# Kernel tuning notes

Measured on AMD Instinct MI355X. Metric: run time of the kernel, lower is better.

## Reference

```python
import jax, jax.numpy as jnp
import numpy as np

DIM = 256
DH = 32
HEADS = DIM // DH
AG = 6      # agent_size
WS = 7      # window_size
N = AG * WS * WS  # 294 tokens per window


def _rel_index():
    ws = (AG, WS, WS)
    coords = np.stack(np.meshgrid(np.arange(ws[0]), np.arange(ws[1]), np.arange(ws[2]), indexing='ij'))
    flat = coords.reshape(3, -1)                      # (3, N)
    rel = flat[:, :, None] - flat[:, None, :]         # (3, N, N)
    rel = rel.transpose(1, 2, 0).copy()               # (N, N, 3)
    rel[..., 0] += ws[0] - 1
    rel[..., 1] += ws[1] - 1
    rel[..., 2] += ws[2] - 1
    rel[..., 0] *= (2 * ws[1] - 1) * (2 * ws[2] - 1)
    rel[..., 1] *= (2 * ws[2] - 1)
    return rel.sum(-1).astype(np.int32)               # (N, N)


def setup_inputs() -> dict:
    key = jax.random.key(0)
    k1, k2, k3, k4, k5 = jax.random.split(key, 5)
    x = jax.random.normal(k1, (1, AG, 16, 16, WS, WS, DIM), dtype=jnp.float32)
    mask = jax.random.randint(k2, (1, 16, 16, WS, WS, 1, AG), 0, 2, dtype=jnp.int32)
    w_qkv = jax.random.normal(k3, (DIM, 3 * DIM), dtype=jnp.float32) * (DIM ** -0.5)
    w_out = jax.random.normal(k4, (DIM, DIM), dtype=jnp.float32) * (DIM ** -0.5)
    n_bias = (2 * AG - 1) * (2 * WS - 1) * (2 * WS - 1)
    bias_table = jax.random.normal(k5, (n_bias, HEADS), dtype=jnp.float32) * 0.02
    rel_index = jnp.asarray(_rel_index())
    return {"x": x, "mask": mask, "w_qkv": w_qkv, "w_out": w_out,
            "bias_table": bias_table, "rel_index": rel_index}


def reference(x, mask, w_qkv, w_out, bias_table, rel_index):
    b, l, gx, gy, w1, w2, d = x.shape
    h, dh = HEADS, DH
    # 'b l x y w1 w2 d -> (b x y) (l w1 w2) d'
    xw = x.transpose(0, 2, 3, 1, 4, 5, 6).reshape(b * gx * gy, l * w1 * w2, d)
    B_, n, _ = xw.shape
    qkv = xw @ w_qkv                                  # (B_, N, 3d)
    q, k, v = jnp.split(qkv, 3, axis=-1)
    # 'b n (h d) -> b h n d'
    q = q.reshape(B_, n, h, dh).transpose(0, 2, 1, 3) * (dh ** -0.5)
    k = k.reshape(B_, n, h, dh).transpose(0, 2, 1, 3)
    v = v.reshape(B_, n, h, dh).transpose(0, 2, 1, 3)
    sim = jnp.einsum('bhid,bhjd->bhij', q, k)         # (B_, h, N, N)
    bias = bias_table[rel_index]                      # (N, N, h)
    sim = sim + bias.transpose(2, 0, 1)[None]
    # 'b x y w1 w2 e l -> (b x y) e (l w1 w2)', then unsqueeze head dim
    m = mask.transpose(0, 1, 2, 5, 6, 3, 4).reshape(B_, -1, n)[:, None]  # (B_,1,e,N)
    sim = jnp.where(m == 0, -jnp.inf, sim)
    attn = jax.nn.softmax(sim, axis=-1)
    out = jnp.einsum('bhij,bhjd->bhid', attn, v)      # (B_, h, N, dh)
    # 'b h (l w1 w2) d -> b l w1 w2 (h d)'
    out = out.transpose(0, 2, 1, 3).reshape(B_, l, w1, w2, h * dh)
    out = out @ w_out
    # '(b x y) l w1 w2 d -> b l x y w1 w2 d'
    return out.reshape(b, gx, gy, l, w1, w2, d).transpose(0, 3, 1, 2, 4, 5, 6)
```

## Files before the change

kernel.cpp:

```cpp
#include <hip/hip_runtime.h>

typedef unsigned short u16;
typedef unsigned int   u32;

#define NTOK 294
#define KS_STRIDE 34
#define VT_STRIDE 300
#define WST 260
#define OBUF_BYTES 38535168ull
#define FLAG_OFF (OBUF_BYTES)

#define ROWS_ALLOC 75280ull
#define BUFB (ROWS_ALLOC * 512ull)
#define QWS_OFF   0ull
#define KWS_OFF   (QWS_OFF + BUFB)
#define VWS_OFF   (KWS_OFF + BUFB)
#define OWS_OFF   (VWS_OFF + BUFB)
#define BIASM_OFF (OWS_OFF + BUFB)
#define WQT_OFF   (BIASM_OFF + 1478656ull)
#define WOT_OFF   (WQT_OFF + 393216ull)
#define FLAG2_OFF (WOT_OFF + 131072ull)
#define NEED_WS   (FLAG2_OFF + 4ull)

typedef __fp16 hv2  __attribute__((ext_vector_type(2)));
typedef __fp16 f16x8 __attribute__((ext_vector_type(8)));
typedef float  f32x4 __attribute__((ext_vector_type(4)));

__device__ __forceinline__ float b2f(u16 v){ union{u32 u; float f;} x; x.u = ((u32)v) << 16; return x.f; }
__device__ __forceinline__ u16 f2b(float f){
  union{float f; u32 u;} x; x.f = f; u32 u = x.u;
  return (u16)((u + 0x7fffu + ((u >> 16) & 1u)) >> 16);
}
__device__ __forceinline__ u32 pack2h(float a, float b){
#if __has_builtin(__builtin_amdgcn_cvt_pkrtz)
  auto r = __builtin_amdgcn_cvt_pkrtz(a, b);
  union{ decltype(r) h; u32 u; } x; x.h = r; return x.u;
#else
  union{ hv2 h; u32 u; } x; x.h[0] = (__fp16)a; x.h[1] = (__fp16)b; return x.u;
#endif
}
__device__ __forceinline__ u32 bfp2h(u32 bfp){
  union{u32 u; float f;} lo, hi; lo.u = bfp << 16; hi.u = bfp & 0xffff0000u;
  return pack2h(lo.f, hi.f);
}
__device__ __forceinline__ u16 f2h(float a){ return (u16)(pack2h(a, 0.0f) & 0xffffu); }

__device__ __forceinline__ float dot2f(u32 a, u32 b, float c){
#if __has_builtin(__builtin_amdgcn_fdot2)
  union{u32 u; hv2 h;} A, B; A.u = a; B.u = b;
  return __builtin_amdgcn_fdot2(A.h, B.h, c, false);
#else
  union{u32 u; __fp16 h[2];} A, B; A.u = a; B.u = b;
  return c + (float)A.h[0]*(float)B.h[0] + (float)A.h[1]*(float)B.h[1];
#endif
}

__device__ __forceinline__ f32x4 mfma16(f16x8 a, f16x8 b, f32x4 c){
  return __builtin_amdgcn_mfma_f32_16x16x32_f16(a, b, c, 0, 0, 0);
}

__device__ __forceinline__ void gl2lds16(const void* g, void* l){
#if __has_builtin(__builtin_amdgcn_global_load_lds)
  __builtin_amdgcn_global_load_lds(
      (const __attribute__((address_space(1))) void*)g,
      (__attribute__((address_space(3))) void*)l, 16, 0, 0);
#else
  *(f16x8*)l = *(const f16x8*)g;
#endif
}

__device__ __forceinline__ void stageB(const u16* __restrict__ wsrc, int nt,
                                       u16* lbase, int wave, int lane){
#pragma unroll
  for (int c = 0; c < 2; ++c){
    int G   = (c*4 + wave)*64 + lane;
    int row = G >> 5, g = G & 31;
    int sg  = g ^ (row & 7);
    const u16* src = wsrc + (size_t)nt*4096 + row*256 + sg*8;
    u16* dst = lbase + (size_t)(c*4 + wave)*512;
    gl2lds16(src, dst);
  }
}

__device__ __forceinline__ f16x8 readB(const u16* bb, int ks, int q, int n16){
  return *(const f16x8*)&bb[n16*256 + (((ks*4 + q) ^ (n16 & 7)) * 8)];
}

__global__ void dfab_probe_kernel(const u16* __restrict__ X, int* __restrict__ flag)
{
  const int lane = threadIdx.x;
  int cnt = 0;
#pragma unroll
  for (int k = 0; k < 8; ++k){
    u16 v = X[lane * 8 + k];
    int e = (v >> 7) & 0xFF;
    cnt += (e < 96 || e > 158) ? 1 : 0;
  }
  for (int off = 32; off > 0; off >>= 1) cnt += __shfl_xor(cnt, off);
  if (lane == 0) *flag = (cnt > 64) ? 1 : 0;
}


__global__ __launch_bounds__(256) void dfab_prep_kernel(
    const void* __restrict__ Wqkvv, const void* __restrict__ Woutv,
    const void* __restrict__ BiasTv, const int* __restrict__ RelIdx,
    u16* __restrict__ wqt, u16* __restrict__ wot, u16* __restrict__ biasm,
    const int* __restrict__ flagp)
{
  const int f32m = *(const volatile int*)flagp;
  const u16* Wb = (const u16*)Wqkvv;  const float* Wf = (const float*)Wqkvv;
  const u16* Ob = (const u16*)Woutv;  const float* Of = (const float*)Woutv;
  const u16* Bb = (const u16*)BiasTv; const float* Bf = (const float*)BiasTv;
  int idx = blockIdx.x * 256 + threadIdx.x;
  if (idx < 196608){
    int n = idx >> 8, k = idx & 255;
    float w = f32m ? Wf[k*768 + n] : b2f(Wb[k*768 + n]);
    if (n < 256) w *= 0.17677669529663687f;
    wqt[n*256 + k] = f2h(w);
  } else if (idx < 262144){
    int t = idx - 196608; int n = t >> 8, k = t & 255;
    float w = f32m ? Of[k*256 + n] : b2f(Ob[k*256 + n]);
    wot[n*256 + k] = f2h(w);
  } else {
    int t = idx - 262144;
    int hh = t / 92416; int rem = t - hh * 92416;
    int j = rem / 304;  int i = rem - j * 304;
    float v = 0.f;
    if (i < NTOK && j < NTOK){
      int nb = RelIdx[i * NTOK + j] * 8 + hh;
      v = f32m ? Bf[nb] : b2f(Bb[nb]);
    }
    biasm[((size_t)(hh*304 + j))*304 + i] = f2h(v);
  }
}

__global__ __launch_bounds__(256, 4) void dfab_qkv_kernel(
    const void* __restrict__ Xv, const u16* __restrict__ wqt,
    u16* __restrict__ Qws, u16* __restrict__ Kws, u16* __restrict__ Vws,
    const int* __restrict__ flagp)
{
  __shared__ __align__(16) union {
    u16 xs[64 * 264];
    struct { u16 bs[2][4096]; u16 cs[4][1024]; } p;
  } sm;

  const int tid = threadIdx.x;
  const int m0 = blockIdx.x * 64;
  const int f32m = *(const volatile int*)flagp;
  const u16* Xb = (const u16*)Xv; const float* Xf = (const float*)Xv;
  const int wave = tid >> 6, lane = tid & 63;
  const int q = lane >> 4, n16 = lane & 15;

  for (int idx = tid; idx < 64 * 128; idx += 256){
    int rl = idx >> 7, d2 = idx & 127;
    int m = m0 + rl; int win = m / 294, tok = m - win * 294;
    int l = tok / 49, r = tok - l * 49;
    size_t src = ((size_t)((l*256 + win)*49 + r))*256 + 2*d2;
    u32 hp;
    if (f32m){ float2 xx = *(const float2*)&Xf[src]; hp = pack2h(xx.x, xx.y); }
    else     { hp = bfp2h(*(const u32*)&Xb[src]); }
    *(u32*)&sm.xs[rl * 264 + 2*d2] = hp;
  }
  __syncthreads();

  f16x8 afr[8];
#pragma unroll
  for (int ks = 0; ks < 8; ++ks)
    afr[ks] = *(const f16x8*)&sm.xs[(wave*16 + n16) * 264 + ks*32 + q*8];
  __syncthreads();

  stageB(wqt, 0, &sm.p.bs[0][0], wave, lane);
  __syncthreads();

  u16* myC = &sm.p.cs[wave][0];
  const size_t rowb = (size_t)(m0 + wave*16);
  const int rbrow = lane >> 3, seg = lane & 7;

#pragma unroll 1
  for (int grp = 0; grp < 12; ++grp){
    u16* dstp = (grp < 4) ? Qws : ((grp < 8) ? Kws : Vws);
    const int g4 = grp & 3;
#pragma unroll
    for (int t = 0; t < 4; ++t){
      const int nt = grp*4 + t;
      if (nt < 47) stageB(wqt, nt+1, &sm.p.bs[(nt+1)&1][0], wave, lane);
      const u16* bb = &sm.p.bs[nt&1][0];
      f16x8 bfr[8];
#pragma unroll
      for (int ks = 0; ks < 8; ++ks) bfr[ks] = readB(bb, ks, q, n16);
      f32x4 c0 = {0.f,0.f,0.f,0.f}, c1 = {0.f,0.f,0.f,0.f};
#pragma unroll
      for (int ks = 0; ks < 4; ++ks){
        c0 = mfma16(afr[ks],     bfr[ks],     c0);
        c1 = mfma16(afr[ks + 4], bfr[ks + 4], c1);
      }
#pragma unroll
      for (int r = 0; r < 4; ++r)
        myC[(q*4 + r)*64 + t*16 + n16] = f2h(c0[r] + c1[r]);
      __syncthreads();
    }
    __asm__ volatile("s_waitcnt lgkmcnt(0)" ::: "memory");
#pragma unroll
    for (int p = 0; p < 2; ++p){
      const int row = p*8 + rbrow;
      f16x8 v = *(const f16x8*)&myC[row*64 + seg*8];
      *(f16x8*)&dstp[(rowb + row)*256 + g4*64 + seg*8] = v;
    }
  }
}

__global__ __launch_bounds__(256, 2) void dfab_attn2_kernel(
    const u16* __restrict__ Qws, const u16* __restrict__ Kws,
    const u16* __restrict__ Vws, const u16* __restrict__ BiasM,
    const int* __restrict__ Mask, u16* __restrict__ Ows)
{
  __shared__ __align__(16) u16 Ks[304 * 40];
  __shared__ __align__(16) u16 Vt[32 * 328];
  __shared__ __align__(16) u16 Pw[4][16 * 168];
  __shared__ float Madd[304];

  const int tid = threadIdx.x;
  const int win = blockIdx.x >> 3, h = blockIdx.x & 7;
  const int wave = tid >> 6, lane = tid & 63;
  const int q = lane >> 4, n16 = lane & 15;

  for (int j = tid; j < 304; j += 256){
    float mv = -1e30f;
    if (j < NTOK){ int l = j / 49, r = j - l * 49;
      mv = (Mask[(win * 49 + r) * 6 + l] != 0) ? 0.0f : -1e30f; }
    Madd[j] = mv;
  }

  {
    const int rr0 = tid >> 2, seg = tid & 3;
#pragma unroll
    for (int p = 0; p < 5; ++p){
      int rr = rr0 + p*64;
      if (rr < NTOK){
        f16x8 kv = *(const f16x8*)&Kws[((size_t)(win*NTOK + rr))*256 + h*32 + seg*8];
        *(f16x8*)&Ks[rr*40 + seg*8] = kv;
      }
    }
    if (tid < 40){
      int rr = NTOK + (tid >> 2);
      uint4 z = {0u,0u,0u,0u};
      *(uint4*)&Ks[rr*40 + seg*8] = z;
    }
#pragma unroll
    for (int p = 0; p < 5; ++p){
      int tok = rr0 + p*64;
      union{ f16x8 h; u16 s[8]; } vv;
      uint4 z = {0u,0u,0u,0u};
      *(uint4*)&vv = z;
      if (tok < NTOK)
        vv.h = *(const f16x8*)&Vws[((size_t)(win*NTOK + tok))*256 + h*32 + seg*8];
      if (tok < 320){
#pragma unroll
        for (int k = 0; k < 8; ++k) Vt[(seg*8 + k)*328 + tok] = vv.s[k];
      }
    }
  }
  __syncthreads();

  float maddv[19];
#pragma unroll
  for (int nt = 0; nt < 19; ++nt) maddv[nt] = Madd[nt*16 + n16];

  u16* myP = Pw[wave];
  int mt = wave;
  f16x8 qf = *(const f16x8*)&Qws[((size_t)(win*NTOK + mt*16 + n16))*256 + h*32 + q*8];

#pragma unroll 1
  for (; mt < 19; mt += 4){
    const int m0 = mt * 16;

    uint2 bu[19];
#pragma unroll
    for (int nt = 0; nt < 19; ++nt)
      bu[nt] = *(const uint2*)&BiasM[((size_t)(h*304 + nt*16 + n16))*304 + m0 + q*4];

    float S[19][4];
#pragma unroll
    for (int nt = 0; nt < 19; ++nt){
      f16x8 kf = *(const f16x8*)&Ks[(nt*16 + n16)*40 + q*8];
      union { uint2 u; __fp16 hh[4]; } b; b.u = bu[nt];
      f32x4 c = { (float)b.hh[0] + maddv[nt], (float)b.hh[1] + maddv[nt],
                  (float)b.hh[2] + maddv[nt], (float)b.hh[3] + maddv[nt] };
      c = mfma16(qf, kf, c);
#pragma unroll
      for (int r = 0; r < 4; ++r) S[nt][r] = c[r];
    }

    const int mtn = mt + 4;
    f16x8 qfn = qf;
    if (mtn < 19)
      qfn = *(const f16x8*)&Qws[((size_t)(win*NTOK + mtn*16 + n16))*256 + h*32 + q*8];

    float rinv[4];
#pragma unroll
    for (int r = 0; r < 4; ++r){
      float mx = S[0][r];
#pragma unroll
      for (int nt = 1; nt < 19; ++nt) mx = fmaxf(mx, S[nt][r]);
      mx = fmaxf(mx, __shfl_xor(mx, 1));
      mx = fmaxf(mx, __shfl_xor(mx, 2));
      mx = fmaxf(mx, __shfl_xor(mx, 4));
      mx = fmaxf(mx, __shfl_xor(mx, 8));
      float sum = 0.f;
#pragma unroll
      for (int nt = 0; nt < 19; ++nt){ float e = __expf(S[nt][r] - mx); S[nt][r] = e; sum += e; }
      sum += __shfl_xor(sum, 1);
      sum += __shfl_xor(sum, 2);
      sum += __shfl_xor(sum, 4);
      sum += __shfl_xor(sum, 8);
      rinv[r] = 1.0f / sum;
    }
    f32x4 o0 = {0.f,0.f,0.f,0.f}, o1 = {0.f,0.f,0.f,0.f};
#pragma unroll
    for (int half = 0; half < 2; ++half){
#pragma unroll
      for (int ntl = 0; ntl < 10; ++ntl){
        int nt = half * 10 + ntl;
        int col = ntl * 16 + n16;
#pragma unroll
        for (int r = 0; r < 4; ++r)
          myP[(q*4 + r) * 168 + col] = (nt < 19) ? f2h(S[nt][r]) : (u16)0;
      }
      __asm__ volatile("s_waitcnt lgkmcnt(0)" ::: "memory");
#pragma unroll
      for (int kk = 0; kk < 5; ++kk){
        f16x8 pf = *(const f16x8*)&myP[n16 * 168 + kk*32 + q*8];
        f16x8 v0 = *(const f16x8*)&Vt[n16 * 328 + half*160 + kk*32 + q*8];
        f16x8 v1 = *(const f16x8*)&Vt[(16 + n16) * 328 + half*160 + kk*32 + q*8];
        o0 = mfma16(pf, v0, o0);
        o1 = mfma16(pf, v1, o1);
      }
      __asm__ volatile("s_waitcnt lgkmcnt(0)" ::: "memory");
    }
#pragma unroll
    for (int r = 0; r < 4; ++r){
      int tok = m0 + q*4 + r;
      if (tok < NTOK){
        size_t base = ((size_t)(win*NTOK + tok))*256 + h*32;
        Ows[base + n16]      = f2h(o0[r] * rinv[r]);
        Ows[base + 16 + n16] = f2h(o1[r] * rinv[r]);
      }
    }
    qf = qfn;
  }
}

__global__ __launch_bounds__(256, 4) void dfab_proj2_kernel(
    const u16* __restrict__ Ows, const u16* __restrict__ wot,
    void* __restrict__ Outv, const int* __restrict__ flagp)
{
  __shared__ __align__(16) u16   Bs[2][4096];
  __shared__ __align__(16) float Csf[4][16 * 64];

  const int tid = threadIdx.x;
  const int wave = tid >> 6, lane = tid & 63;
  const int q = lane >> 4, n16 = lane & 15;
  const int mr = blockIdx.x * 64 + wave * 16;
  const int f32m = *(const volatile int*)flagp;

  stageB(wot, 0, &Bs[0][0], wave, lane);

  f16x8 afr[8];
#pragma unroll
  for (int ks = 0; ks < 8; ++ks)
    afr[ks] = *(const f16x8*)&Ows[((size_t)(mr + n16))*256 + ks*32 + q*8];

  const int rbrow = lane >> 3, seg = lane & 7;
  size_t ob0, ob1;
  {
    int m = mr + rbrow;     int win = m / 294, tok = m - win*294;
    int l = tok / 49, rr = tok - l*49;
    ob0 = ((size_t)((l*256 + win)*49 + rr))*256;
    m = mr + 8 + rbrow;     win = m / 294; tok = m - win*294;
    l = tok / 49; rr = tok - l*49;
    ob1 = ((size_t)((l*256 + win)*49 + rr))*256;
  }

  float* myC = &Csf[wave][0];
  __syncthreads();

#pragma unroll 1
  for (int g4 = 0; g4 < 4; ++g4){
#pragma unroll
    for (int t = 0; t < 4; ++t){
      const int nt = g4*4 + t;
      if (nt < 15) stageB(wot, nt+1, &Bs[(nt+1)&1][0], wave, lane);
      const u16* bb = &Bs[nt&1][0];
      f16x8 bfr[8];
#pragma unroll
      for (int ks = 0; ks < 8; ++ks) bfr[ks] = readB(bb, ks, q, n16);
      f32x4 c0 = {0.f,0.f,0.f,0.f}, c1 = {0.f,0.f,0.f,0.f};
#pragma unroll
      for (int ks = 0; ks < 4; ++ks){
        c0 = mfma16(afr[ks],     bfr[ks],     c0);
        c1 = mfma16(afr[ks + 4], bfr[ks + 4], c1);
      }
#pragma unroll
      for (int r = 0; r < 4; ++r)
        myC[(q*4 + r)*64 + t*16 + n16] = c0[r] + c1[r];
      __syncthreads();
    }
    __asm__ volatile("s_waitcnt lgkmcnt(0)" ::: "memory");
#pragma unroll
    for (int p = 0; p < 2; ++p){
      const int row = p*8 + rbrow;
      const size_t ob = p ? ob1 : ob0;
      f32x4 v0 = *(const f32x4*)&myC[row*64 + seg*8];
      f32x4 v1 = *(const f32x4*)&myC[row*64 + seg*8 + 4];
      if (f32m){
        *(f32x4*)&((float*)Outv)[ob + g4*64 + seg*8]     = v0;
        *(f32x4*)&((float*)Outv)[ob + g4*64 + seg*8 + 4] = v1;
      } else {
        union{ u32 w[4]; u16 h[8]; } pk;
        pk.h[0]=f2b(v0[0]); pk.h[1]=f2b(v0[1]); pk.h[2]=f2b(v0[2]); pk.h[3]=f2b(v0[3]);
        pk.h[4]=f2b(v1[0]); pk.h[5]=f2b(v1[1]); pk.h[6]=f2b(v1[2]); pk.h[7]=f2b(v1[3]);
        *(uint4*)&((u16*)Outv)[ob + g4*64 + seg*8] = *(const uint4*)&pk.w[0];
      }
    }
  }
}

__global__ __launch_bounds__(256) void dfab_attn_kernel(
    const void* __restrict__ Xv, const int* __restrict__ Mask,
    const void* __restrict__ Wqkvv, const void* __restrict__ BiasTv,
    const int* __restrict__ RelIdx, u16* __restrict__ Obuf,
    const int* __restrict__ flagp)
{
  __shared__ __align__(16) char lds[59736];
  u16* Ks   = (u16*)(lds);
  u16* Vt   = (u16*)(lds + 19992);
  u16* Wp   = (u16*)(lds + 39192);
  u16* Xs   = (u16*)(lds + 47512);
  u16* Wqt  = (u16*)(lds + 39192);
  u32* Pb   = (u32*)(lds + 55832);
  float* Madd = (float*)(lds + 58264);
  u16* Qb   = (u16*)(lds + 59480);

  const int tid = threadIdx.x;
  const int bx  = blockIdx.x;
  const int win = bx >> 3, h = bx & 7;

  const int f32m = *(const volatile int*)flagp;
  const u16*   Xb = (const u16*)Xv;       const float* Xf = (const float*)Xv;
  const u16*   Wb = (const u16*)Wqkvv;    const float* Wf = (const float*)Wqkvv;
  const u16*   Bb = (const u16*)BiasTv;   const float* Bf = (const float*)BiasTv;

  for (int j = tid; j < 304; j += 256){
    float mv = -1e30f;
    if (j < NTOK){ int l = j / 49, r = j - l * 49;
      mv = (Mask[(win * 49 + r) * 6 + l] != 0) ? 0.0f : -1e30f; }
    Madd[j] = mv;
  }
  for (int idx = tid; idx < 32 * 6; idx += 256){
    int c = idx / 6; Vt[c * VT_STRIDE + NTOK + (idx - c * 6)] = 0;
  }

#pragma unroll 1
  for (int p = 0; p < 4; ++p){
    const int kind = p >> 1;
    const int colbase = 256 + kind * 256 + h * 32 + (p & 1) * 16;
    __syncthreads();
    for (int idx = tid; idx < 16 * 128; idx += 256){
      int c = idx & 15, d2 = idx >> 4;
      float w0, w1;
      if (f32m){ w0 = Wf[(2 * d2) * 768 + colbase + c]; w1 = Wf[(2 * d2 + 1) * 768 + colbase + c]; }
      else     { w0 = b2f(Wb[(2 * d2) * 768 + colbase + c]); w1 = b2f(Wb[(2 * d2 + 1) * 768 + colbase + c]); }
      *(u32*)&Wp[c * WST + 2 * d2] = pack2h(w0, w1);
    }
#pragma unroll 1
    for (int jt = 0; jt < 19; ++jt){
      const int j0 = jt * 16;
      const int nj = (NTOK - j0 < 16) ? (NTOK - j0) : 16;
      __syncthreads();
      for (int idx = tid; idx < nj * 128; idx += 256){
        int jl = idx >> 7, d2 = idx & 127;
        int tok = j0 + jl; int l = tok / 49, r = tok - l * 49;
        size_t off = (size_t)((l * 256 + win) * 49 + r) * 256 + 2 * d2;
        u32 hp;
        if (f32m){ float2 xx = *(const float2*)&Xf[off]; hp = pack2h(xx.x, xx.y); }
        else     { hp = bfp2h(*(const u32*)&Xb[off]); }
        *(u32*)&Xs[jl * WST + 2 * d2] = hp;
      }
      __syncthreads();
      const int jl = tid >> 4, c = tid & 15;
      const u32* xp = (const u32*)&Xs[jl * WST];
      const u32* wp = (const u32*)&Wp[c * WST];
      float a0 = 0.f, a1 = 0.f;
#pragma unroll 4
      for (int d2 = 0; d2 < 128; d2 += 4){
        uint2 xa = *(const uint2*)(xp + d2), xb = *(const uint2*)(xp + d2 + 2);
        uint2 wa = *(const uint2*)(wp + d2), wb = *(const uint2*)(wp + d2 + 2);
        a0 = dot2f(xa.x, wa.x, a0); a1 = dot2f(xa.y, wa.y, a1);
        a0 = dot2f(xb.x, wb.x, a0); a1 = dot2f(xb.y, wb.y, a1);
      }
      if (jl < nj){
        u16 hv = f2h(a0 + a1);
        int tok = j0 + jl;
        if (kind == 0) Ks[tok * KS_STRIDE + (p & 1) * 16 + c] = hv;
        else           Vt[((p & 1) * 16 + c) * VT_STRIDE + tok] = hv;
      }
    }
  }
  __syncthreads();
  for (int idx = tid; idx < 32 * 128; idx += 256){
    int c = idx & 31, d2 = idx >> 5;
    float w0, w1;
    if (f32m){ w0 = Wf[(2 * d2) * 768 + h * 32 + c]; w1 = Wf[(2 * d2 + 1) * 768 + h * 32 + c]; }
    else     { w0 = b2f(Wb[(2 * d2) * 768 + h * 32 + c]); w1 = b2f(Wb[(2 * d2 + 1) * 768 + h * 32 + c]); }
    *(u32*)&Wqt[c * WST + 2 * d2] = pack2h(w0, w1);
  }
  __syncthreads();

  const int wave = tid >> 6, lane = tid & 63;
  const int hf = lane >> 5, c32 = lane & 31;
  u32* mypb = Pb + wave * 152;
  u16* qbw  = Qb + wave * 32;

  for (int i = wave; i < NTOK; i += 4){
    const int li = i / 49, ri = i - li * 49;
    const size_t rowoff = (size_t)((li * 256 + win) * 49 + ri) * 256;
    const u32* wqp = (const u32*)&Wqt[c32 * WST];
    float q0 = 0.f, q1 = 0.f;
    if (f32m){
      const float4* xr4 = (const float4*)&Xf[rowoff];
#pragma unroll 4
      for (int d2 = hf * 64; d2 < hf * 64 + 64; d2 += 2){
        uint2 wq = *(const uint2*)(wqp + d2);
        float4 xx = xr4[d2 >> 1];
        q0 = dot2f(pack2h(xx.x, xx.y), wq.x, q0);
        q1 = dot2f(pack2h(xx.z, xx.w), wq.y, q1);
      }
    } else {
      const u32* xr = (const u32*)&Xb[rowoff];
#pragma unroll 4
      for (int d2 = hf * 64; d2 < hf * 64 + 64; d2 += 2){
        uint2 wq = *(const uint2*)(wqp + d2);
        q0 = dot2f(bfp2h(xr[d2]),     wq.x, q0);
        q1 = dot2f(bfp2h(xr[d2 + 1]), wq.y, q1);
      }
    }
    float qa = q0 + q1;
    qa += __shfl_xor(qa, 32);
    if (hf == 0) qbw[c32] = f2h(qa * 0.17677669529663687f);
    __asm__ volatile("s_waitcnt lgkmcnt(0)" ::: "memory");
    u32 qp[16];
#pragma unroll
    for (int cc = 0; cc < 16; ++cc) qp[cc] = *(const u32*)&qbw[2 * cc];

    float sv[5];
#pragma unroll
    for (int it = 0; it < 5; ++it){
      int j = it * 64 + lane;
      float a;
      if (j < NTOK){
        int nb = RelIdx[i * NTOK + j] * 8 + h;
        float bias = f32m ? Bf[nb] : b2f(Bb[nb]);
        float a0 = bias + Madd[j];
        float a1 = 0.f;
        const u16* kr = &Ks[j * KS_STRIDE];
#pragma unroll
        for (int cc = 0; cc < 16; cc += 2){
          a0 = dot2f(qp[cc],     *(const u32*)&kr[2 * cc],     a0);
          a1 = dot2f(qp[cc + 1], *(const u32*)&kr[2 * cc + 2], a1);
        }
        a = a0 + a1;
      } else a = -3e38f;
      sv[it] = a;
    }
    float m = sv[0];
#pragma unroll
    for (int it = 1; it < 5; ++it) m = fmaxf(m, sv[it]);
    for (int off = 32; off > 0; off >>= 1) m = fmaxf(m, __shfl_xor(m, off));
    float lsum = 0.f;
#pragma unroll
    for (int it = 0; it < 5; ++it){ float e = __expf(sv[it] - m); sv[it] = e; lsum += e; }
    for (int off = 32; off > 0; off >>= 1) lsum += __shfl_xor(lsum, off);
    const float rinv = 1.0f / lsum;
#pragma unroll
    for (int it = 0; it < 5; ++it){
      float pn = sv[it] * rinv;
      float po = __shfl_xor(pn, 1);
      int j = it * 64 + lane;
      if (!(lane & 1) && j < 304) mypb[j >> 1] = pack2h(pn, po);
    }
    __asm__ volatile("s_waitcnt lgkmcnt(0)" ::: "memory");
    const u16* vr = &Vt[c32 * VT_STRIDE];
    const int jb = hf * 148;
    float o0 = 0.f, o1 = 0.f;
#pragma unroll 4
    for (int g = 0; g < 37; ++g){
      int j = jb + 4 * g;
      uint2 vv = *(const uint2*)&vr[j];
      uint2 pp = *(const uint2*)&mypb[j >> 1];
      o0 = dot2f(pp.x, vv.x, o0);
      o1 = dot2f(pp.y, vv.y, o1);
    }
    float o = o0 + o1;
    o += __shfl_xor(o, 32);
    if (hf == 0)
      Obuf[(size_t)(win * NTOK + i) * 256 + h * 32 + c32] = f2b(o);
  }
}

__global__ __launch_bounds__(256) void dfab_proj_kernel(
    const u16* __restrict__ Obuf, const void* __restrict__ Woutv,
    void* __restrict__ Outv, const int* __restrict__ flagp)
{
  __shared__ __align__(16) char lds[33920];
  u16* Ot = (u16*)(lds);
  u16* Wt = (u16*)(lds + 16512);

  const int tid = threadIdx.x;
  const int bx = blockIdx.x;
  const int win = bx / 10, tile = bx - win * 10;
  const int t0 = tile * 32;
  const int nt = (NTOK - t0 < 32) ? (NTOK - t0) : 32;

  const int f32m = *(const volatile int*)flagp;
  const u16* Wob = (const u16*)Woutv; const float* Wof = (const float*)Woutv;

  for (int idx = tid; idx < nt * 128; idx += 256){
    int t = idx >> 7, k2 = idx & 127;
    u32 oo = *(const u32*)&Obuf[(size_t)(win * NTOK + t0 + t) * 256 + 2 * k2];
    *(u32*)&Ot[t * 258 + 2 * k2] = bfp2h(oo);
  }

  float acc[32];
#pragma unroll
  for (int t = 0; t < 32; ++t) acc[t] = 0.f;
  const int dd = tid;

#pragma unroll 1
  for (int kt = 0; kt < 8; ++kt){
    __syncthreads();
    for (int idx = tid; idx < 4096; idx += 256){
      int d = idx & 255, kk2 = idx >> 8;
      int k = kt * 32 + 2 * kk2;
      float w0, w1;
      if (f32m){ w0 = Wof[k * 256 + d]; w1 = Wof[(k + 1) * 256 + d]; }
      else     { w0 = b2f(Wob[k * 256 + d]); w1 = b2f(Wob[(k + 1) * 256 + d]); }
      *(u32*)&Wt[d * 34 + 2 * kk2] = pack2h(w0, w1);
    }
    __syncthreads();
#pragma unroll 2
    for (int kk2 = 0; kk2 < 16; ++kk2){
      u32 wp = *(const u32*)&Wt[dd * 34 + 2 * kk2];
      const u16* orow = &Ot[kt * 32 + 2 * kk2];
#pragma unroll 8
      for (int t = 0; t < 32; ++t){
        u32 op = *(const u32*)&orow[t * 258];
        acc[t] = dot2f(op, wp, acc[t]);
      }
    }
  }

  for (int t = 0; t < nt; ++t){
    int tok = t0 + t; int l = tok / 49, r = tok - l * 49;
    size_t oidx = (size_t)((l * 256 + win) * 49 + r) * 256 + dd;
    if (f32m) ((float*)Outv)[oidx] = acc[t];
    else      ((u16*)Outv)[oidx]   = f2b(acc[t]);
  }
}

extern "C" void kernel_launch(void* const* d_in, const int* in_sizes, int n_in,
                              void* d_out, int out_size, void* d_ws, size_t ws_size,
                              hipStream_t stream) {
  (void)in_sizes; (void)n_in; (void)out_size;
  const void* x          = d_in[0];
  const int*  mask       = (const int*)d_in[1];
  const void* w_qkv      = d_in[2];
  const void* w_out      = d_in[3];
  const void* bias_table = d_in[4];
  const int*  rel_index  = (const int*)d_in[5];
  char* ws = (char*)d_ws;

  if (ws_size >= NEED_WS){
    u16* qws   = (u16*)(ws + QWS_OFF);
    u16* kws   = (u16*)(ws + KWS_OFF);
    u16* vws   = (u16*)(ws + VWS_OFF);
    u16* ows   = (u16*)(ws + OWS_OFF);
    u16* biasm = (u16*)(ws + BIASM_OFF);
    u16* wqt   = (u16*)(ws + WQT_OFF);
    u16* wot   = (u16*)(ws + WOT_OFF);
    int* flag  = (int*)(ws + FLAG2_OFF);
    dfab_probe_kernel<<<1, 64, 0, stream>>>((const u16*)x, flag);
    dfab_prep_kernel<<<3912, 256, 0, stream>>>(w_qkv, w_out, bias_table, rel_index,
                                               wqt, wot, biasm, flag);
    dfab_qkv_kernel<<<1176, 256, 0, stream>>>(x, wqt, qws, kws, vws, flag);
    dfab_attn2_kernel<<<2048, 256, 0, stream>>>(qws, kws, vws, biasm, mask, ows);
    dfab_proj2_kernel<<<1176, 256, 0, stream>>>(ows, wot, d_out, flag);
  } else {
    u16* obuf = (u16*)ws;
    int* flag = (int*)(ws + FLAG_OFF);
    dfab_probe_kernel<<<1, 64, 0, stream>>>((const u16*)x, flag);
    dfab_attn_kernel<<<2048, 256, 0, stream>>>(x, mask, w_qkv, bias_table, rel_index, obuf, flag);
    dfab_proj_kernel<<<2560, 256, 0, stream>>>(obuf, w_out, d_out, flag);
  }
}
```

Baseline: 367.2 us.

## Hold K fragments in registers, fold log2e into scales, use exp2 softmax

Drops the K shared-memory tile: each lane loads its 19 K fragments straight from global into registers, cutting LDS use and a staging pass. The mask becomes a per-lane bitmask that selects -1e30 instead of adding a float, and log2(e) is folded into the Q scale and the bias table so softmax can call the native exp2. The max and sum reductions are split into independent chains for more instruction-level parallelism. In exchange, register pressure rises by about 76 VGPRs for the K fragments, which may hurt occupancy under launch_bounds(256,2), and bias loads now sit inside the tile loop instead of being issued ahead.

```diff
diff --git a/kernel.cpp b/kernel.cpp
--- a/kernel.cpp
+++ b/kernel.cpp
@@ -52,6 +52,14 @@
 #else
   union{u32 u; __fp16 h[2];} A, B; A.u = a; B.u = b;
   return c + (float)A.h[0]*(float)B.h[0] + (float)A.h[1]*(float)B.h[1];
+#endif
+}
+
+__device__ __forceinline__ float fexp2(float x){
+#if __has_builtin(__builtin_amdgcn_exp2f)
+  return __builtin_amdgcn_exp2f(x);
+#else
+  return exp2f(x);
 #endif
 }
 
@@ -115,7 +123,7 @@
   if (idx < 196608){
     int n = idx >> 8, k = idx & 255;
     float w = f32m ? Wf[k*768 + n] : b2f(Wb[k*768 + n]);
-    if (n < 256) w *= 0.17677669529663687f;
+    if (n < 256) w *= 0.25503487f;
     wqt[n*256 + k] = f2h(w);
   } else if (idx < 262144){
     int t = idx - 196608; int n = t >> 8, k = t & 255;
@@ -129,6 +137,7 @@
     if (i < NTOK && j < NTOK){
       int nb = RelIdx[i * NTOK + j] * 8 + hh;
       v = f32m ? Bf[nb] : b2f(Bb[nb]);
+      v *= 1.4426950409f;
     }
     biasm[((size_t)(hh*304 + j))*304 + i] = f2h(v);
   }
@@ -214,7 +223,6 @@
     const u16* __restrict__ Vws, const u16* __restrict__ BiasM,
     const int* __restrict__ Mask, u16* __restrict__ Ows)
 {
-  __shared__ __align__(16) u16 Ks[304 * 40];
   __shared__ __align__(16) u16 Vt[32 * 328];
   __shared__ __align__(16) u16 Pw[4][16 * 168];
   __shared__ float Madd[304];
@@ -233,19 +241,6 @@
 
   {
     const int rr0 = tid >> 2, seg = tid & 3;
-#pragma unroll
-    for (int p = 0; p < 5; ++p){
-      int rr = rr0 + p*64;
-      if (rr < NTOK){
-        f16x8 kv = *(const f16x8*)&Kws[((size_t)(win*NTOK + rr))*256 + h*32 + seg*8];
-        *(f16x8*)&Ks[rr*40 + seg*8] = kv;
-      }
-    }
-    if (tid < 40){
-      int rr = NTOK + (tid >> 2);
-      uint4 z = {0u,0u,0u,0u};
-      *(uint4*)&Ks[rr*40 + seg*8] = z;
-    }
 #pragma unroll
     for (int p = 0; p < 5; ++p){
       int tok = rr0 + p*64;
@@ -262,9 +257,21 @@
   }
   __syncthreads();
 
-  float maddv[19];
-#pragma unroll
-  for (int nt = 0; nt < 19; ++nt) maddv[nt] = Madd[nt*16 + n16];
+  f16x8 kf[19];
+#pragma unroll
+  for (int nt = 0; nt < 19; ++nt){
+    int tok = nt*16 + n16;
+    union{ f16x8 h; uint4 u; } kv;
+    uint4 z = {0u,0u,0u,0u}; kv.u = z;
+    if (tok < NTOK)
+      kv.h = *(const f16x8*)&Kws[((size_t)(win*NTOK + tok))*256 + h*32 + q*8];
+    kf[nt] = kv.h;
+  }
+
+  u32 mbits = 0;
+#pragma unroll
+  for (int nt = 0; nt < 19; ++nt)
+    if (Madd[nt*16 + n16] < -1e29f) mbits |= (1u << nt);
 
   u16* myP = Pw[wave];
   int mt = wave;
@@ -274,19 +281,16 @@
   for (; mt < 19; mt += 4){
     const int m0 = mt * 16;
 
-    uint2 bu[19];
-#pragma unroll
-    for (int nt = 0; nt < 19; ++nt)
-      bu[nt] = *(const uint2*)&BiasM[((size_t)(h*304 + nt*16 + n16))*304 + m0 + q*4];
-
     float S[19][4];
 #pragma unroll
     for (int nt = 0; nt < 19; ++nt){
-      f16x8 kf = *(const f16x8*)&Ks[(nt*16 + n16)*40 + q*8];
-      union { uint2 u; __fp16 hh[4]; } b; b.u = bu[nt];
-      f32x4 c = { (float)b.hh[0] + maddv[nt], (float)b.hh[1] + maddv[nt],
-                  (float)b.hh[2] + maddv[nt], (float)b.hh[3] + maddv[nt] };
-      c = mfma16(qf, kf, c);
+      union { uint2 u; __fp16 hh[4]; } b;
+      b.u = *(const uint2*)&BiasM[((size_t)(h*304 + nt*16 + n16))*304 + m0 + q*4];
+      const bool mk = (mbits >> nt) & 1u;
+      f32x4 c;
+#pragma unroll
+      for (int r = 0; r < 4; ++r) c[r] = mk ? -1e30f : (float)b.hh[r];
+      c = mfma16(qf, kf[nt], c);
 #pragma unroll
       for (int r = 0; r < 4; ++r) S[nt][r] = c[r];
     }
@@ -299,16 +303,29 @@
     float rinv[4];
 #pragma unroll
     for (int r = 0; r < 4; ++r){
-      float mx = S[0][r];
-#pragma unroll
-      for (int nt = 1; nt < 19; ++nt) mx = fmaxf(mx, S[nt][r]);
+      float a0 = fmaxf(fmaxf(S[0][r],  S[1][r]),  S[2][r]);
+      float a1 = fmaxf(fmaxf(S[3][r],  S[4][r]),  S[5][r]);
+      float a2 = fmaxf(fmaxf(S[6][r],  S[7][r]),  S[8][r]);
+      float a3 = fmaxf(fmaxf(S[9][r],  S[10][r]), S[11][r]);
+      float a4 = fmaxf(fmaxf(S[12][r], S[13][r]), S[14][r]);
+      float a5 = fmaxf(fmaxf(S[15][r], S[16][r]), S[17][r]);
+      float mx = fmaxf(fmaxf(fmaxf(a0, a1), fmaxf(a2, a3)),
+                       fmaxf(fmaxf(a4, a5), S[18][r]));
       mx = fmaxf(mx, __shfl_xor(mx, 1));
       mx = fmaxf(mx, __shfl_xor(mx, 2));
       mx = fmaxf(mx, __shfl_xor(mx, 4));
       mx = fmaxf(mx, __shfl_xor(mx, 8));
-      float sum = 0.f;
-#pragma unroll
-      for (int nt = 0; nt < 19; ++nt){ float e = __expf(S[nt][r] - mx); S[nt][r] = e; sum += e; }
+      float s0 = 0.f, s1 = 0.f, s2 = 0.f, s3 = 0.f;
+#pragma unroll
+      for (int nt = 0; nt < 19; ++nt){
+        float e = fexp2(S[nt][r] - mx);
+        S[nt][r] = e;
+        if ((nt & 3) == 0) s0 += e;
+        else if ((nt & 3) == 1) s1 += e;
+        else if ((nt & 3) == 2) s2 += e;
+        else s3 += e;
+      }
+      float sum = (s0 + s1) + (s2 + s3);
       sum += __shfl_xor(sum, 1);
       sum += __shfl_xor(sum, 2);
       sum += __shfl_xor(sum, 4);
```

Result: slower. 498.8 us (+35.9%).
